# Performance work log

Measured on AMD Instinct MI355X. Metric: run time of the kernel, lower is better.

Reference implementation:

```python
import jax, jax.numpy as jnp
import numpy as np
import math

B, S, D = 1, 4096, 2048
H, KVH, HD = 32, 8, 64
W = 512            # sliding window size (== block size)
THETA = 10000.0
EPS = 1e-5
INTER = 5632
PRE_SCALE = 1.0 / math.sqrt(2.0)


def setup_inputs() -> dict:
    key = jax.random.key(0)
    ks = jax.random.split(key, 8)
    def w(k, shape, fan_in):
        return jax.random.normal(k, shape, jnp.float32) * (fan_in ** -0.5)
    return {
        "hidden_states": jax.random.normal(ks[0], (B, S, D), jnp.float32),
        "mixer_norm_w": jnp.ones((D,), jnp.float32),
        "wq": w(ks[1], (D, H * HD), D),
        "wk": w(ks[2], (D, KVH * HD), D),
        "wv": w(ks[3], (D, KVH * HD), D),
        "wo": w(ks[4], (H * HD, D), H * HD),
        "mlp_norm_w": jnp.ones((D,), jnp.float32),
        "w_gate": w(ks[5], (D, 2 * INTER), D),
        "w_down": w(ks[6], (INTER, D), INTER),
    }


def rmsnorm(x, w, eps=EPS):
    return x * jax.lax.rsqrt(jnp.mean(x * x, axis=-1, keepdims=True) + eps) * w


def rope(x):
    # x: [B, S, h, HD]; rotate-half RoPE
    half = HD // 2
    inv_freq = 1.0 / (THETA ** (jnp.arange(0, HD, 2, dtype=jnp.float32) / HD))
    freqs = jnp.arange(S, dtype=jnp.float32)[:, None] * inv_freq[None, :]  # [S, half]
    cos = jnp.cos(freqs)[None, :, None, :]
    sin = jnp.sin(freqs)[None, :, None, :]
    x1, x2 = x[..., :half], x[..., half:]
    return jnp.concatenate([x1 * cos - x2 * sin, x2 * cos + x1 * sin], axis=-1)


def sliding_attention(x, wq, wk, wv, wo):
    # x already pre-scaled; returns attn output (pre /pre_scale)
    q = (x @ wq).reshape(B, S, H, HD)
    k = (x @ wk).reshape(B, S, KVH, HD)
    v = (x @ wv).reshape(B, S, KVH, HD)
    q, k = rope(q), rope(k)
    rep = H // KVH
    k = jnp.repeat(k, rep, axis=2)  # [B,S,H,HD]
    v = jnp.repeat(v, rep, axis=2)
    nb = S // W
    qb = q.reshape(B, nb, W, H, HD)
    kb = k.reshape(B, nb, W, H, HD)
    vb = v.reshape(B, nb, W, H, HD)
    zeros = jnp.zeros((B, 1, W, H, HD), q.dtype)
    kw = jnp.concatenate([jnp.concatenate([zeros, kb[:, :-1]], axis=1), kb], axis=2)  # [B,nb,2W,H,HD]
    vw = jnp.concatenate([jnp.concatenate([zeros, vb[:, :-1]], axis=1), vb], axis=2)
    # local mask [nb, W, 2W]
    blk = jnp.arange(nb)[:, None, None]
    q_pos = blk * W + jnp.arange(W)[None, :, None]
    k_pos = blk * W - W + jnp.arange(2 * W)[None, None, :]
    mask = (k_pos >= 0) & (k_pos <= q_pos) & (q_pos - k_pos < W)
    scores = jnp.einsum("bnqhd,bnkhd->bhnqk", qb, kw) * (HD ** -0.5)
    scores = jnp.where(mask[None, None], scores, jnp.finfo(scores.dtype).min)
    p = jax.nn.softmax(scores, axis=-1)
    out = jnp.einsum("bhnqk,bnkhd->bnqhd", p, vw).reshape(B, S, H * HD)
    return out @ wo


def reference(hidden_states, mixer_norm_w, wq, wk, wv, wo, mlp_norm_w, w_gate, w_down):
    residual = hidden_states
    x = rmsnorm(hidden_states, mixer_norm_w)
    attn_out = sliding_attention(x * PRE_SCALE, wq, wk, wv, wo) / PRE_SCALE
    h = residual + attn_out
    xn = rmsnorm(h, mlp_norm_w)
    gv = xn @ w_gate
    gate, y = gv[..., :INTER], gv[..., INTER:]
    mlp_out = (jax.nn.silu(gate) * y) @ w_down
    return h + mlp_out
```

## Files before the change

### kernel.cpp

```cpp
#include <hip/hip_runtime.h>
#include <stdint.h>

typedef __attribute__((ext_vector_type(8))) short s16x8;
typedef __attribute__((ext_vector_type(4))) float f32x4;

#define GLD_LDS16(gp, lp) __builtin_amdgcn_global_load_lds( \
    (__attribute__((address_space(1))) void*)(void*)(gp), \
    (__attribute__((address_space(3))) void*)(lp), 16, 0, 0)

__device__ __forceinline__ float b2f(unsigned short s) {
    unsigned int u = ((unsigned int)s) << 16;
    return __builtin_bit_cast(float, u);
}
__device__ __forceinline__ unsigned short f2b(float f) {
    unsigned int u = __builtin_bit_cast(unsigned int, f);
    u = (u + 0x7FFFu + ((u >> 16) & 1u)) >> 16;
    return (unsigned short)u;
}
__device__ __forceinline__ f32x4 mfma16(s16x8 a, s16x8 b, f32x4 c) {
    return __builtin_amdgcn_mfma_f32_16x16x32_bf16(a, b, c, 0, 0, 0);
}

__global__ __launch_bounds__(256) void rmsnorm_bf16(
    const float* __restrict__ x, const float* __restrict__ wgt,
    unsigned short* __restrict__ out)
{
    const int row = blockIdx.x;
    const int t = threadIdx.x;
    const float* xr = x + (size_t)row * 2048;
    float4 a = *(const float4*)(xr + t * 8);
    float4 b = *(const float4*)(xr + t * 8 + 4);
    float ss = a.x*a.x + a.y*a.y + a.z*a.z + a.w*a.w
             + b.x*b.x + b.y*b.y + b.z*b.z + b.w*b.w;
    #pragma unroll
    for (int d = 1; d < 64; d <<= 1) ss += __shfl_xor(ss, d);
    __shared__ float red[4];
    if ((t & 63) == 0) red[t >> 6] = ss;
    __syncthreads();
    float tot = red[0] + red[1] + red[2] + red[3];
    float inv = rsqrtf(tot * (1.0f / 2048.0f) + 1e-5f);
    float vals[8] = {a.x, a.y, a.z, a.w, b.x, b.y, b.z, b.w};
    const float* wr_ = wgt + t * 8;
    s16x8 ov;
    #pragma unroll
    for (int j = 0; j < 8; ++j) ov[j] = (short)f2b(vals[j] * inv * wr_[j]);
    *(s16x8*)(out + (size_t)row * 2048 + t * 8) = ov;
}

__global__ __launch_bounds__(256) void transpose_to_bf16(
    const float* __restrict__ in, unsigned short* __restrict__ out, int K, int N)
{
    __shared__ float tile[64][65];
    const int n0 = blockIdx.x * 64, k0 = blockIdx.y * 64;
    const int t = threadIdx.x;
    const int kr = t >> 4, nc = (t & 15) * 4;
    #pragma unroll
    for (int i = 0; i < 4; ++i) {
        float4 v = *(const float4*)(in + (size_t)(k0 + kr + i * 16) * N + n0 + nc);
        tile[nc + 0][kr + i * 16] = v.x;
        tile[nc + 1][kr + i * 16] = v.y;
        tile[nc + 2][kr + i * 16] = v.z;
        tile[nc + 3][kr + i * 16] = v.w;
    }
    __syncthreads();
    const int nr = t >> 3, kc = (t & 7) * 8;
    #pragma unroll
    for (int p = 0; p < 2; ++p) {
        s16x8 o;
        #pragma unroll
        for (int j = 0; j < 8; ++j) o[j] = (short)f2b(tile[nr + p * 32][kc + j]);
        *(s16x8*)(out + (size_t)(n0 + nr + p * 32) * K + k0 + kc) = o;
    }
}

template <int BN, int EPI>
__global__ __launch_bounds__(512, 2) void gemmq(
    const unsigned short* __restrict__ A,
    const unsigned short* __restrict__ B,
    void* __restrict__ Cv,
    const float* __restrict__ ADD,
    int N, int K)
{
    constexpr int WN  = BN / 4;
    constexpr int HN  = WN / 2;
    constexpr int NJQ = WN / 32;
    constexpr int NBU = BN / 64;
    constexpr int ABUF = 256 * 64;
    constexpr int BBUF = BN * 64;
    __shared__ __align__(16) unsigned short As[2 * ABUF];
    __shared__ __align__(16) unsigned short Bs[2 * BBUF];

    const int t = threadIdx.x;
    const int l = t & 63, w = t >> 6;
    const int l15 = l & 15, lg = l >> 4;
    const int wr = w >> 2, wc = w & 3;
    const int x7 = l15 & 7;
    const int cc0 = ((lg) ^ x7) << 3;
    const int cc1 = ((4 | lg) ^ x7) << 3;

    const int nwg = (int)gridDim.x;
    const int orig = (int)blockIdx.x;
    const int q8 = nwg >> 3, r8 = nwg & 7;
    const int xcd = orig & 7, lid = orig >> 3;
    const int wg = (xcd < r8 ? xcd * (q8 + 1) : r8 * (q8 + 1) + (xcd - r8) * q8) + lid;
    const int m0 = (wg & 15) * 256;
    const int n0 = (wg >> 4) * BN;

    const int tr = t >> 3;
    const int scol = ((t & 7) ^ (tr & 7)) << 3;
    const unsigned short* pA[4];
    #pragma unroll
    for (int u = 0; u < 4; ++u) {
        const int lrow = u * 64 + tr;
        const int g = ((lrow >> 6) & 1) * 128 + (lrow >> 7) * 64 + (lrow & 63);
        pA[u] = A + (size_t)(m0 + g) * K + scol;
    }
    const unsigned short* pB[NBU];
    #pragma unroll
    for (int u = 0; u < NBU; ++u) {
        const int lrow = u * 64 + tr;
        const int h = lrow / (BN / 2), rem = lrow % (BN / 2);
        const int g = (rem / HN) * WN + h * HN + (rem % HN);
        pB[u] = B + (size_t)(n0 + g) * K + scol;
    }

    f32x4 acc[2][2][4][NJQ] = {};
    s16x8 aF[4][2];
    s16x8 bF[2][NJQ][2];

    const int NT = K / 64;

    #pragma unroll
    for (int u = 0; u < 4; ++u) GLD_LDS16(pA[u], &As[u * 4096 + t * 8]);
    #pragma unroll
    for (int u = 0; u < NBU; ++u) GLD_LDS16(pB[u], &Bs[u * 4096 + t * 8]);
    asm volatile("s_waitcnt vmcnt(0)" ::: "memory");
    __builtin_amdgcn_s_barrier();

    for (int kt = 0; kt < NT; ++kt) {
        const int rb  = (kt & 1) ? ABUF : 0;
        const int rbB = (kt & 1) ? BBUF : 0;
        const int wb  = ABUF - rb;
        const int wbB = BBUF - rbB;
        const int knext = (kt + 1 < NT ? kt + 1 : kt) * 64;

        #pragma unroll
        for (int i = 0; i < 4; ++i) {
            const int lr = wr * 64 + i * 16 + l15;
            aF[i][0] = *(const s16x8*)&As[rb + lr * 64 + cc0];
            aF[i][1] = *(const s16x8*)&As[rb + lr * 64 + cc1];
        }
        #pragma unroll
        for (int j = 0; j < NJQ; ++j) {
            const int lr = wc * HN + j * 16 + l15;
            bF[0][j][0] = *(const s16x8*)&Bs[rbB + lr * 64 + cc0];
            bF[0][j][1] = *(const s16x8*)&Bs[rbB + lr * 64 + cc1];
        }
        #pragma unroll
        for (int u = 0; u < 4; ++u)
            GLD_LDS16(pA[u] + knext, &As[wb + u * 4096 + t * 8]);
        __builtin_amdgcn_s_setprio(1);
        #pragma unroll
        for (int kk = 0; kk < 2; ++kk)
            #pragma unroll
            for (int i = 0; i < 4; ++i)
                #pragma unroll
                for (int j = 0; j < NJQ; ++j)
                    acc[0][0][i][j] = mfma16(aF[i][kk], bF[0][j][kk], acc[0][0][i][j]);
        __builtin_amdgcn_s_setprio(0);

        #pragma unroll
        for (int j = 0; j < NJQ; ++j) {
            const int lr = (BN / 2) + wc * HN + j * 16 + l15;
            bF[1][j][0] = *(const s16x8*)&Bs[rbB + lr * 64 + cc0];
            bF[1][j][1] = *(const s16x8*)&Bs[rbB + lr * 64 + cc1];
        }
        #pragma unroll
        for (int u = 0; u < NBU; ++u)
            GLD_LDS16(pB[u] + knext, &Bs[wbB + u * 4096 + t * 8]);
        __builtin_amdgcn_s_setprio(1);
        #pragma unroll
        for (int kk = 0; kk < 2; ++kk)
            #pragma unroll
            for (int i = 0; i < 4; ++i)
                #pragma unroll
                for (int j = 0; j < NJQ; ++j)
                    acc[0][1][i][j] = mfma16(aF[i][kk], bF[1][j][kk], acc[0][1][i][j]);
        __builtin_amdgcn_s_setprio(0);

        #pragma unroll
        for (int i = 0; i < 4; ++i) {
            const int lr = 128 + wr * 64 + i * 16 + l15;
            aF[i][0] = *(const s16x8*)&As[rb + lr * 64 + cc0];
            aF[i][1] = *(const s16x8*)&As[rb + lr * 64 + cc1];
        }
        __builtin_amdgcn_s_setprio(1);
        #pragma unroll
        for (int kk = 0; kk < 2; ++kk)
            #pragma unroll
            for (int i = 0; i < 4; ++i)
                #pragma unroll
                for (int j = 0; j < NJQ; ++j)
                    acc[1][0][i][j] = mfma16(aF[i][kk], bF[0][j][kk], acc[1][0][i][j]);
        __builtin_amdgcn_s_setprio(0);

        __builtin_amdgcn_s_setprio(1);
        #pragma unroll
        for (int kk = 0; kk < 2; ++kk)
            #pragma unroll
            for (int i = 0; i < 4; ++i)
                #pragma unroll
                for (int j = 0; j < NJQ; ++j)
                    acc[1][1][i][j] = mfma16(aF[i][kk], bF[1][j][kk], acc[1][1][i][j]);
        __builtin_amdgcn_s_setprio(0);

        asm volatile("s_waitcnt vmcnt(0)" ::: "memory");
        __builtin_amdgcn_s_barrier();
    }

    #pragma unroll
    for (int qm = 0; qm < 2; ++qm)
        #pragma unroll
        for (int i = 0; i < 4; ++i)
            #pragma unroll
            for (int r = 0; r < 4; ++r) {
                const int row = m0 + wr * 128 + qm * 64 + i * 16 + lg * 4 + r;
                const size_t rbase = (size_t)row * N;
                #pragma unroll
                for (int qn = 0; qn < 2; ++qn)
                    #pragma unroll
                    for (int j = 0; j < NJQ; ++j) {
                        const int col = n0 + wc * WN + qn * HN + j * 16 + l15;
                        float v = acc[qm][qn][i][j][r];
                        if constexpr (EPI == 0) {
                            ((unsigned short*)Cv)[rbase + col] = f2b(v);
                        } else {
                            ((float*)Cv)[rbase + col] = v + ADD[rbase + col];
                        }
                    }
            }
}

__global__ __launch_bounds__(512, 2) void gemm_glu(
    const unsigned short* __restrict__ A,
    const unsigned short* __restrict__ Bg,
    const unsigned short* __restrict__ By,
    unsigned short* __restrict__ act,
    int N, int K)
{
    constexpr int ABUF = 256 * 64, BBUF = 128 * 64;
    __shared__ __align__(16) unsigned short As[2 * ABUF];
    __shared__ __align__(16) unsigned short Bgs[2 * BBUF];
    __shared__ __align__(16) unsigned short Bys[2 * BBUF];

    const int t = threadIdx.x;
    const int l = t & 63, w = t >> 6;
    const int l15 = l & 15, lg = l >> 4;
    const int wr = w >> 2, wc = w & 3;
    const int x7 = l15 & 7;
    const int cc0 = ((lg) ^ x7) << 3;
    const int cc1 = ((4 | lg) ^ x7) << 3;

    const int nwg = (int)gridDim.x;
    const int orig = (int)blockIdx.x;
    const int q8 = nwg >> 3;
    const int xcd = orig & 7, lid = orig >> 3;
    const int wg = xcd * q8 + lid;
    const int m0 = (wg & 15) * 256;
    const int n0 = (wg >> 4) * 128;

    const int tr = t >> 3;
    const int scol = ((t & 7) ^ (tr & 7)) << 3;
    const unsigned short* pA[4];
    #pragma unroll
    for (int u = 0; u < 4; ++u) {
        const int lrow = u * 64 + tr;
        const int g = ((lrow >> 6) & 1) * 128 + (lrow >> 7) * 64 + (lrow & 63);
        pA[u] = A + (size_t)(m0 + g) * K + scol;
    }
    const unsigned short *pG[2], *pY[2];
    #pragma unroll
    for (int u = 0; u < 2; ++u) {
        const int g = (tr >> 4) * 32 + u * 16 + (tr & 15);
        pG[u] = Bg + (size_t)(n0 + g) * K + scol;
        pY[u] = By + (size_t)(n0 + g) * K + scol;
    }

    f32x4 accG[2][2][4] = {};
    f32x4 accY[2][2][4] = {};
    s16x8 aF[4][2];
    s16x8 gF[2][2], yF[2][2];

    const int NT = K / 64;

    #pragma unroll
    for (int u = 0; u < 4; ++u) GLD_LDS16(pA[u], &As[u * 4096 + t * 8]);
    GLD_LDS16(pG[0], &Bgs[0 * 4096 + t * 8]);
    GLD_LDS16(pY[0], &Bys[0 * 4096 + t * 8]);
    GLD_LDS16(pG[1], &Bgs[1 * 4096 + t * 8]);
    GLD_LDS16(pY[1], &Bys[1 * 4096 + t * 8]);
    asm volatile("s_waitcnt vmcnt(0)" ::: "memory");
    __builtin_amdgcn_s_barrier();

    for (int kt = 0; kt < NT; ++kt) {
        const int rb  = (kt & 1) ? ABUF : 0;
        const int rbB = (kt & 1) ? BBUF : 0;
        const int wb  = ABUF - rb;
        const int wbB = BBUF - rbB;
        const int knext = (kt + 1 < NT ? kt + 1 : kt) * 64;

        #pragma unroll
        for (int i = 0; i < 4; ++i) {
            const int lr = wr * 64 + i * 16 + l15;
            aF[i][0] = *(const s16x8*)&As[rb + lr * 64 + cc0];
            aF[i][1] = *(const s16x8*)&As[rb + lr * 64 + cc1];
        }
        {
            const int lr = wc * 16 + l15;
            gF[0][0] = *(const s16x8*)&Bgs[rbB + lr * 64 + cc0];
            gF[0][1] = *(const s16x8*)&Bgs[rbB + lr * 64 + cc1];
            yF[0][0] = *(const s16x8*)&Bys[rbB + lr * 64 + cc0];
            yF[0][1] = *(const s16x8*)&Bys[rbB + lr * 64 + cc1];
        }
        #pragma unroll
        for (int u = 0; u < 4; ++u)
            GLD_LDS16(pA[u] + knext, &As[wb + u * 4096 + t * 8]);
        __builtin_amdgcn_s_setprio(1);
        #pragma unroll
        for (int kk = 0; kk < 2; ++kk)
            #pragma unroll
            for (int i = 0; i < 4; ++i) {
                accG[0][0][i] = mfma16(aF[i][kk], gF[0][kk], accG[0][0][i]);
                accY[0][0][i] = mfma16(aF[i][kk], yF[0][kk], accY[0][0][i]);
            }
        __builtin_amdgcn_s_setprio(0);

        {
            const int lr = 64 + wc * 16 + l15;
            gF[1][0] = *(const s16x8*)&Bgs[rbB + lr * 64 + cc0];
            gF[1][1] = *(const s16x8*)&Bgs[rbB + lr * 64 + cc1];
            yF[1][0] = *(const s16x8*)&Bys[rbB + lr * 64 + cc0];
            yF[1][1] = *(const s16x8*)&Bys[rbB + lr * 64 + cc1];
        }
        GLD_LDS16(pG[0] + knext, &Bgs[wbB + 0 * 4096 + t * 8]);
        GLD_LDS16(pY[0] + knext, &Bys[wbB + 0 * 4096 + t * 8]);
        GLD_LDS16(pG[1] + knext, &Bgs[wbB + 1 * 4096 + t * 8]);
        GLD_LDS16(pY[1] + knext, &Bys[wbB + 1 * 4096 + t * 8]);
        __builtin_amdgcn_s_setprio(1);
        #pragma unroll
        for (int kk = 0; kk < 2; ++kk)
            #pragma unroll
            for (int i = 0; i < 4; ++i) {
                accG[0][1][i] = mfma16(aF[i][kk], gF[1][kk], accG[0][1][i]);
                accY[0][1][i] = mfma16(aF[i][kk], yF[1][kk], accY[0][1][i]);
            }
        __builtin_amdgcn_s_setprio(0);

        #pragma unroll
        for (int i = 0; i < 4; ++i) {
            const int lr = 128 + wr * 64 + i * 16 + l15;
            aF[i][0] = *(const s16x8*)&As[rb + lr * 64 + cc0];
            aF[i][1] = *(const s16x8*)&As[rb + lr * 64 + cc1];
        }
        __builtin_amdgcn_s_setprio(1);
        #pragma unroll
        for (int kk = 0; kk < 2; ++kk)
            #pragma unroll
            for (int i = 0; i < 4; ++i) {
                accG[1][0][i] = mfma16(aF[i][kk], gF[0][kk], accG[1][0][i]);
                accY[1][0][i] = mfma16(aF[i][kk], yF[0][kk], accY[1][0][i]);
            }
        __builtin_amdgcn_s_setprio(0);

        __builtin_amdgcn_s_setprio(1);
        #pragma unroll
        for (int kk = 0; kk < 2; ++kk)
            #pragma unroll
            for (int i = 0; i < 4; ++i) {
                accG[1][1][i] = mfma16(aF[i][kk], gF[1][kk], accG[1][1][i]);
                accY[1][1][i] = mfma16(aF[i][kk], yF[1][kk], accY[1][1][i]);
            }
        __builtin_amdgcn_s_setprio(0);

        asm volatile("s_waitcnt vmcnt(0)" ::: "memory");
        __builtin_amdgcn_s_barrier();
    }

    #pragma unroll
    for (int qm = 0; qm < 2; ++qm)
        #pragma unroll
        for (int i = 0; i < 4; ++i)
            #pragma unroll
            for (int r = 0; r < 4; ++r) {
                const int row = m0 + wr * 128 + qm * 64 + i * 16 + lg * 4 + r;
                const size_t rbase = (size_t)row * N;
                #pragma unroll
                for (int qn = 0; qn < 2; ++qn) {
                    const int col = n0 + wc * 32 + qn * 16 + l15;
                    float g = accG[qm][qn][i][r];
                    float y = accY[qm][qn][i][r];
                    float sg = g / (1.0f + expf(-g));
                    act[rbase + col] = f2b(sg * y);
                }
            }
}

__global__ void rope_tab_k(float2* __restrict__ tab) {
    int i = blockIdx.x * 256 + threadIdx.x;
    if (i >= 4096 * 32) return;
    int s = i >> 5, d = i & 31;
    float inv = exp2f(-(float)d * (13.287712379549449f / 32.0f));
    float fr = (float)s * inv;
    float sv, cv;
    sincosf(fr, &sv, &cv);
    tab[i] = make_float2(cv, sv);
}

__global__ void rope_apply_k(unsigned short* __restrict__ qkv, const float2* __restrict__ tab) {
    int i = blockIdx.x * 256 + threadIdx.x;
    if (i >= 4096 * 40 * 4) return;
    int dg = i & 3;
    int rest = i >> 2;
    int head = rest % 40;
    int s = rest / 40;
    int off = head < 32 ? head * 64 : 2048 + (head - 32) * 64;
    unsigned short* p = qkv + (size_t)s * 3072 + off + dg * 8;
    s16x8 x1 = *(const s16x8*)p;
    s16x8 x2 = *(const s16x8*)(p + 32);
    const float2* tb = tab + s * 32 + dg * 8;
    s16x8 o1, o2;
    #pragma unroll
    for (int j = 0; j < 8; ++j) {
        float2 cs = tb[j];
        float a = b2f((unsigned short)x1[j]);
        float b = b2f((unsigned short)x2[j]);
        o1[j] = (short)f2b(a * cs.x - b * cs.y);
        o2[j] = (short)f2b(b * cs.x + a * cs.y);
    }
    *(s16x8*)p = o1;
    *(s16x8*)(p + 32) = o2;
}

__global__ __launch_bounds__(256) void attn_swa(
    const unsigned short* __restrict__ qkv,
    unsigned short* __restrict__ out)
{
    constexpr int LDQ = 3072;
    const int qb = blockIdx.x;
    const int h = blockIdx.y;
    const int kvh = h >> 2;
    const int q0 = qb * 64;
    const int t = threadIdx.x, l = t & 63, w = t >> 6;
    const int l15 = l & 15, lg = l >> 4;

    __shared__ unsigned short Kl[64 * 64];
    __shared__ unsigned short Vt[64 * 72];
    __shared__ unsigned short Pl[4 * 16 * 72];

    s16x8 qf[2];
    {
        const unsigned short* qp = qkv + (size_t)(q0 + w * 16 + l15) * LDQ + h * 64 + lg * 8;
        qf[0] = *(const s16x8*)(qp);
        qf[1] = *(const s16x8*)(qp + 32);
    }
    float m_run[4] = {-1e30f, -1e30f, -1e30f, -1e30f};
    float l_run[4] = {0.f, 0.f, 0.f, 0.f};
    f32x4 o[4] = {};

    const float SC = 0.0625f * 1.4426950408889634f;
    const int kt_lo = qb >= 8 ? qb - 8 : 0;

    for (int kt = kt_lo; kt <= qb; ++kt) {
        const int ks = kt * 64;
        __syncthreads();
        {
            const unsigned short* kg = qkv + (size_t)(ks + (t >> 3)) * LDQ + 2048 + kvh * 64 + (t & 7) * 8;
            GLD_LDS16(kg, Kl + t * 8);
            GLD_LDS16(kg + (size_t)32 * LDQ, Kl + t * 8 + 2048);
        }
        {
            const unsigned short* vg = qkv + (size_t)(ks + l) * LDQ + 2560 + kvh * 64 + w * 16;
            s16x8 v0 = *(const s16x8*)vg;
            s16x8 v1 = *(const s16x8*)(vg + 8);
            #pragma unroll
            for (int j = 0; j < 8; ++j) Vt[(w * 16 + j) * 72 + l] = (unsigned short)v0[j];
            #pragma unroll
            for (int j = 0; j < 8; ++j) Vt[(w * 16 + 8 + j) * 72 + l] = (unsigned short)v1[j];
        }
        __syncthreads();

        f32x4 sf[4] = {};
        #pragma unroll
        for (int kf = 0; kf < 4; ++kf) {
            #pragma unroll
            for (int kk = 0; kk < 2; ++kk) {
                s16x8 kb = *(const s16x8*)(Kl + (kf * 16 + l15) * 64 + kk * 32 + lg * 8);
                sf[kf] = mfma16(qf[kk], kb, sf[kf]);
            }
        }

        float tmax[4];
        #pragma unroll
        for (int r = 0; r < 4; ++r) {
            int qrow = q0 + w * 16 + lg * 4 + r;
            float mx = -1e30f;
            #pragma unroll
            for (int kf = 0; kf < 4; ++kf) {
                int key = ks + kf * 16 + l15;
                bool valid = (key <= qrow) && (qrow - key < 512);
                if (valid) mx = fmaxf(mx, sf[kf][r]);
            }
            #pragma unroll
            for (int d2 = 1; d2 < 16; d2 <<= 1) mx = fmaxf(mx, __shfl_xor(mx, d2));
            tmax[r] = mx;
        }

        float alpha[4], rsum[4];
        #pragma unroll
        for (int r = 0; r < 4; ++r) {
            float mnew = fmaxf(m_run[r], tmax[r]);
            alpha[r] = exp2f((m_run[r] - mnew) * SC);
            m_run[r] = mnew;
            rsum[r] = 0.f;
        }

        unsigned short* Pw = Pl + w * (16 * 72);
        #pragma unroll
        for (int kf = 0; kf < 4; ++kf) {
            #pragma unroll
            for (int r = 0; r < 4; ++r) {
                int qrow = q0 + w * 16 + lg * 4 + r;
                int key = ks + kf * 16 + l15;
                bool valid = (key <= qrow) && (qrow - key < 512);
                float p = valid ? exp2f((sf[kf][r] - m_run[r]) * SC) : 0.f;
                rsum[r] += p;
                Pw[(lg * 4 + r) * 72 + kf * 16 + l15] = f2b(p);
            }
        }
        #pragma unroll
        for (int r = 0; r < 4; ++r) {
            #pragma unroll
            for (int d2 = 1; d2 < 16; d2 <<= 1) rsum[r] += __shfl_xor(rsum[r], d2);
            l_run[r] = l_run[r] * alpha[r] + rsum[r];
        }
        #pragma unroll
        for (int hf = 0; hf < 4; ++hf)
            #pragma unroll
            for (int r = 0; r < 4; ++r) o[hf][r] *= alpha[r];

        asm volatile("s_waitcnt lgkmcnt(0)" ::: "memory");
        __builtin_amdgcn_sched_barrier(0);

        #pragma unroll
        for (int kk2 = 0; kk2 < 2; ++kk2) {
            s16x8 pa = *(const s16x8*)(Pw + l15 * 72 + kk2 * 32 + lg * 8);
            #pragma unroll
            for (int hf = 0; hf < 4; ++hf) {
                s16x8 vb = *(const s16x8*)(Vt + (hf * 16 + l15) * 72 + kk2 * 32 + lg * 8);
                o[hf] = mfma16(pa, vb, o[hf]);
            }
        }
    }

    #pragma unroll
    for (int r = 0; r < 4; ++r) {
        int qrow = q0 + w * 16 + lg * 4 + r;
        float invl = 1.0f / l_run[r];
        unsigned short* orow = out + (size_t)qrow * 2048 + h * 64;
        #pragma unroll
        for (int hf = 0; hf < 4; ++hf)
            orow[hf * 16 + l15] = f2b(o[hf][r] * invl);
    }
}

extern "C" void kernel_launch(void* const* d_in, const int* in_sizes, int n_in,
                              void* d_out, int out_size, void* d_ws, size_t ws_size,
                              hipStream_t stream)
{
    const float* hidden = (const float*)d_in[0];
    const float* w_mix  = (const float*)d_in[1];
    const float* wq     = (const float*)d_in[2];
    const float* wk     = (const float*)d_in[3];
    const float* wv     = (const float*)d_in[4];
    const float* wo     = (const float*)d_in[5];
    const float* w_mlp  = (const float*)d_in[6];
    const float* wg     = (const float*)d_in[7];
    const float* wd     = (const float*)d_in[8];
    float* out = (float*)d_out;

    char* ws = (char*)d_ws;
    size_t off = 0;
    auto alloc = [&](size_t bytes) {
        char* p = ws + off;
        off += (bytes + 255) & ~(size_t)255;
        return p;
    };
    unsigned short* Wt   = (unsigned short*)alloc((size_t)11264 * 2048 * 2);
    unsigned short* xn   = (unsigned short*)alloc((size_t)4096 * 2048 * 2);
    unsigned short* qkv  = (unsigned short*)alloc((size_t)4096 * 3072 * 2);
    float2*         rtab = (float2*)alloc((size_t)4096 * 32 * 8);
    unsigned short* attn = (unsigned short*)alloc((size_t)4096 * 2048 * 2);
    float*          hbuf = (float*)alloc((size_t)4096 * 2048 * 4);
    unsigned short* act  = (unsigned short*)alloc((size_t)4096 * 5632 * 2);

    rmsnorm_bf16<<<4096, 256, 0, stream>>>(hidden, w_mix, xn);

    transpose_to_bf16<<<dim3(32, 32), 256, 0, stream>>>(wq, Wt, 2048, 2048);
    transpose_to_bf16<<<dim3(8, 32), 256, 0, stream>>>(wk, Wt + (size_t)2048 * 2048, 2048, 512);
    transpose_to_bf16<<<dim3(8, 32), 256, 0, stream>>>(wv, Wt + (size_t)2560 * 2048, 2048, 512);

    gemmq<256, 0><<<192, 512, 0, stream>>>(xn, Wt, qkv, nullptr, 3072, 2048);

    rope_tab_k<<<(4096 * 32 + 255) / 256, 256, 0, stream>>>(rtab);
    rope_apply_k<<<(4096 * 40 * 4 + 255) / 256, 256, 0, stream>>>(qkv, rtab);

    attn_swa<<<dim3(64, 32), 256, 0, stream>>>(qkv, attn);

    transpose_to_bf16<<<dim3(32, 32), 256, 0, stream>>>(wo, Wt, 2048, 2048);
    gemmq<128, 1><<<256, 512, 0, stream>>>(attn, Wt, hbuf, hidden, 2048, 2048);

    rmsnorm_bf16<<<4096, 256, 0, stream>>>(hbuf, w_mlp, xn);

    transpose_to_bf16<<<dim3(176, 32), 256, 0, stream>>>(wg, Wt, 2048, 11264);
    gemm_glu<<<704, 512, 0, stream>>>(xn, Wt, Wt + (size_t)5632 * 2048, act, 5632, 2048);

    transpose_to_bf16<<<dim3(32, 88), 256, 0, stream>>>(wd, Wt, 5632, 2048);
    gemmq<128, 1><<<256, 512, 0, stream>>>(act, Wt, out, hbuf, 2048, 5632);
}
```

Baseline: 534.1 us.

## Fuse RoPE into QKV GEMM epilogue, double-buffer attention K/V, drop setprio

RoPE is now applied in the QKV GEMM epilogue, where each warp holds matching halves of a head (column d and d+32). This removes the separate rope_apply pass over the qkv buffer. The sliding-window attention kernel double-buffers its K/V shared-memory tiles and prefetches the next tile while computing the current one. All s_setprio wrappers around the MFMA blocks in the GEMMs are removed. The costs are extra shared memory in attention and possibly different wave scheduling in the GEMMs without priority hints.

```diff
diff --git a/kernel.cpp b/kernel.cpp
--- a/kernel.cpp
+++ b/kernel.cpp
@@ -79,6 +79,7 @@
     const unsigned short* __restrict__ B,
     void* __restrict__ Cv,
     const float* __restrict__ ADD,
+    const float2* __restrict__ RT,
     int N, int K)
 {
     constexpr int WN  = BN / 4;
@@ -159,7 +160,6 @@
         #pragma unroll
         for (int u = 0; u < 4; ++u)
             GLD_LDS16(pA[u] + knext, &As[wb + u * 4096 + t * 8]);
-        __builtin_amdgcn_s_setprio(1);
         #pragma unroll
         for (int kk = 0; kk < 2; ++kk)
             #pragma unroll
@@ -167,7 +167,6 @@
                 #pragma unroll
                 for (int j = 0; j < NJQ; ++j)
                     acc[0][0][i][j] = mfma16(aF[i][kk], bF[0][j][kk], acc[0][0][i][j]);
-        __builtin_amdgcn_s_setprio(0);
 
         #pragma unroll
         for (int j = 0; j < NJQ; ++j) {
@@ -178,7 +177,6 @@
         #pragma unroll
         for (int u = 0; u < NBU; ++u)
             GLD_LDS16(pB[u] + knext, &Bs[wbB + u * 4096 + t * 8]);
-        __builtin_amdgcn_s_setprio(1);
         #pragma unroll
         for (int kk = 0; kk < 2; ++kk)
             #pragma unroll
@@ -186,7 +184,6 @@
                 #pragma unroll
                 for (int j = 0; j < NJQ; ++j)
                     acc[0][1][i][j] = mfma16(aF[i][kk], bF[1][j][kk], acc[0][1][i][j]);
-        __builtin_amdgcn_s_setprio(0);
 
         #pragma unroll
         for (int i = 0; i < 4; ++i) {
@@ -194,7 +191,6 @@
             aF[i][0] = *(const s16x8*)&As[rb + lr * 64 + cc0];
             aF[i][1] = *(const s16x8*)&As[rb + lr * 64 + cc1];
         }
-        __builtin_amdgcn_s_setprio(1);
         #pragma unroll
         for (int kk = 0; kk < 2; ++kk)
             #pragma unroll
@@ -202,9 +198,7 @@
                 #pragma unroll
                 for (int j = 0; j < NJQ; ++j)
                     acc[1][0][i][j] = mfma16(aF[i][kk], bF[0][j][kk], acc[1][0][i][j]);
-        __builtin_amdgcn_s_setprio(0);
-
-        __builtin_amdgcn_s_setprio(1);
+
         #pragma unroll
         for (int kk = 0; kk < 2; ++kk)
             #pragma unroll
@@ -212,33 +206,61 @@
                 #pragma unroll
                 for (int j = 0; j < NJQ; ++j)
                     acc[1][1][i][j] = mfma16(aF[i][kk], bF[1][j][kk], acc[1][1][i][j]);
-        __builtin_amdgcn_s_setprio(0);
 
         asm volatile("s_waitcnt vmcnt(0)" ::: "memory");
         __builtin_amdgcn_s_barrier();
     }
 
-    #pragma unroll
-    for (int qm = 0; qm < 2; ++qm)
-        #pragma unroll
-        for (int i = 0; i < 4; ++i)
-            #pragma unroll
-            for (int r = 0; r < 4; ++r) {
-                const int row = m0 + wr * 128 + qm * 64 + i * 16 + lg * 4 + r;
-                const size_t rbase = (size_t)row * N;
+    if constexpr (EPI == 2) {
+        unsigned short* Cb = (unsigned short*)Cv;
+        const bool roped = (n0 < 2560);
+        #pragma unroll
+        for (int qm = 0; qm < 2; ++qm)
+            #pragma unroll
+            for (int i = 0; i < 4; ++i)
                 #pragma unroll
-                for (int qn = 0; qn < 2; ++qn)
+                for (int r = 0; r < 4; ++r) {
+                    const int row = m0 + wr * 128 + qm * 64 + i * 16 + lg * 4 + r;
+                    const size_t rbase = (size_t)row * N;
                     #pragma unroll
                     for (int j = 0; j < NJQ; ++j) {
-                        const int col = n0 + wc * WN + qn * HN + j * 16 + l15;
-                        float v = acc[qm][qn][i][j][r];
-                        if constexpr (EPI == 0) {
-                            ((unsigned short*)Cv)[rbase + col] = f2b(v);
+                        const int d = j * 16 + l15;
+                        const int c0 = n0 + wc * WN + j * 16 + l15;
+                        float a = acc[qm][0][i][j][r];
+                        float b = acc[qm][1][i][j][r];
+                        if (roped) {
+                            float2 cs = RT[row * 32 + d];
+                            Cb[rbase + c0]      = f2b(a * cs.x - b * cs.y);
+                            Cb[rbase + c0 + HN] = f2b(b * cs.x + a * cs.y);
                         } else {
-                            ((float*)Cv)[rbase + col] = v + ADD[rbase + col];
+                            Cb[rbase + c0]      = f2b(a);
+                            Cb[rbase + c0 + HN] = f2b(b);
                         }
                     }
-            }
+                }
+    } else {
+        #pragma unroll
+        for (int qm = 0; qm < 2; ++qm)
+            #pragma unroll
+            for (int i = 0; i < 4; ++i)
+                #pragma unroll
+                for (int r = 0; r < 4; ++r) {
+                    const int row = m0 + wr * 128 + qm * 64 + i * 16 + lg * 4 + r;
+                    const size_t rbase = (size_t)row * N;
+                    #pragma unroll
+                    for (int qn = 0; qn < 2; ++qn)
+                        #pragma unroll
+                        for (int j = 0; j < NJQ; ++j) {
+                            const int col = n0 + wc * WN + qn * HN + j * 16 + l15;
+                            float v = acc[qm][qn][i][j][r];
+                            if constexpr (EPI == 0) {
+                                ((unsigned short*)Cv)[rbase + col] = f2b(v);
+                            } else {
+                                ((float*)Cv)[rbase + col] = v + ADD[rbase + col];
+                            }
+                        }
+                }
+    }
 }
 
 __global__ __launch_bounds__(512, 2) void gemm_glu(
@@ -325,7 +347,6 @@
         #pragma unroll
         for (int u = 0; u < 4; ++u)
             GLD_LDS16(pA[u] + knext, &As[wb + u * 4096 + t * 8]);
-        __builtin_amdgcn_s_setprio(1);
         #pragma unroll
         for (int kk = 0; kk < 2; ++kk)
             #pragma unroll
@@ -333,7 +354,6 @@
                 accG[0][0][i] = mfma16(aF[i][kk], gF[0][kk], accG[0][0][i]);
                 accY[0][0][i] = mfma16(aF[i][kk], yF[0][kk], accY[0][0][i]);
             }
-        __builtin_amdgcn_s_setprio(0);
 
         {
             const int lr = 64 + wc * 16 + l15;
@@ -346,7 +366,6 @@
         GLD_LDS16(pY[0] + knext, &Bys[wbB + 0 * 4096 + t * 8]);
         GLD_LDS16(pG[1] + knext, &Bgs[wbB + 1 * 4096 + t * 8]);
         GLD_LDS16(pY[1] + knext, &Bys[wbB + 1 * 4096 + t * 8]);
-        __builtin_amdgcn_s_setprio(1);
         #pragma unroll
         for (int kk = 0; kk < 2; ++kk)
             #pragma unroll
@@ -354,7 +373,6 @@
                 accG[0][1][i] = mfma16(aF[i][kk], gF[1][kk], accG[0][1][i]);
                 accY[0][1][i] = mfma16(aF[i][kk], yF[1][kk], accY[0][1][i]);
             }
-        __builtin_amdgcn_s_setprio(0);
 
         #pragma unroll
         for (int i = 0; i < 4; ++i) {
@@ -362,7 +380,6 @@
             aF[i][0] = *(const s16x8*)&As[rb + lr * 64 + cc0];
             aF[i][1] = *(const s16x8*)&As[rb + lr * 64 + cc1];
         }
-        __builtin_amdgcn_s_setprio(1);
         #pragma unroll
         for (int kk = 0; kk < 2; ++kk)
             #pragma unroll
@@ -370,9 +387,7 @@
                 accG[1][0][i] = mfma16(aF[i][kk], gF[0][kk], accG[1][0][i]);
                 accY[1][0][i] = mfma16(aF[i][kk], yF[0][kk], accY[1][0][i]);
             }
-        __builtin_amdgcn_s_setprio(0);
-
-        __builtin_amdgcn_s_setprio(1);
+
         #pragma unroll
         for (int kk = 0; kk < 2; ++kk)
             #pragma unroll
@@ -380,7 +395,6 @@
                 accG[1][1][i] = mfma16(aF[i][kk], gF[1][kk], accG[1][1][i]);
                 accY[1][1][i] = mfma16(aF[i][kk], yF[1][kk], accY[1][1][i]);
             }
-        __builtin_amdgcn_s_setprio(0);
 
         asm volatile("s_waitcnt vmcnt(0)" ::: "memory");
         __builtin_amdgcn_s_barrier();
@@ -416,31 +430,6 @@
     tab[i] = make_float2(cv, sv);
 }
 
-__global__ void rope_apply_k(unsigned short* __restrict__ qkv, const float2* __restrict__ tab) {
-    int i = blockIdx.x * 256 + threadIdx.x;
-    if (i >= 4096 * 40 * 4) return;
-    int dg = i & 3;
-    int rest = i >> 2;
-    int head = rest % 40;
-    int s = rest / 40;
-    int off = head < 32 ? head * 64 : 2048 + (head - 32) * 64;
-    unsigned short* p = qkv + (size_t)s * 3072 + off + dg * 8;
-    s16x8 x1 = *(const s16x8*)p;
-    s16x8 x2 = *(const s16x8*)(p + 32);
-    const float2* tb = tab + s * 32 + dg * 8;
-    s16x8 o1, o2;
-    #pragma unroll
-    for (int j = 0; j < 8; ++j) {
-        float2 cs = tb[j];
-        float a = b2f((unsigned short)x1[j]);
-        float b = b2f((unsigned short)x2[j]);
-        o1[j] = (short)f2b(a * cs.x - b * cs.y);
-        o2[j] = (short)f2b(b * cs.x + a * cs.y);
-    }
-    *(s16x8*)p = o1;
-    *(s16x8*)(p + 32) = o2;
-}
-
 __global__ __launch_bounds__(256) void attn_swa(
     const unsigned short* __restrict__ qkv,
     unsigned short* __restrict__ out)
@@ -453,8 +442,8 @@
     const int t = threadIdx.x, l = t & 63, w = t >> 6;
     const int l15 = l & 15, lg = l >> 4;
 
-    __shared__ unsigned short Kl[64 * 64];
-    __shared__ unsigned short Vt[64 * 72];
+    __shared__ unsigned short Kl[2][64 * 64];
+    __shared__ unsigned short Vt[2][64 * 72];
     __shared__ unsigned short Pl[4 * 16 * 72];
 
     s16x8 qf[2];
@@ -470,31 +459,45 @@
     const float SC = 0.0625f * 1.4426950408889634f;
     const int kt_lo = qb >= 8 ? qb - 8 : 0;
 
+    {
+        const int ks = kt_lo * 64;
+        const unsigned short* kg = qkv + (size_t)(ks + (t >> 3)) * LDQ + 2048 + kvh * 64 + (t & 7) * 8;
+        GLD_LDS16(kg, &Kl[0][t * 8]);
+        GLD_LDS16(kg + (size_t)32 * LDQ, &Kl[0][t * 8 + 2048]);
+        const unsigned short* vg = qkv + (size_t)(ks + l) * LDQ + 2560 + kvh * 64 + w * 16;
+        s16x8 v0 = *(const s16x8*)vg;
+        s16x8 v1 = *(const s16x8*)(vg + 8);
+        #pragma unroll
+        for (int j = 0; j < 8; ++j) Vt[0][(w * 16 + j) * 72 + l] = (unsigned short)v0[j];
+        #pragma unroll
+        for (int j = 0; j < 8; ++j) Vt[0][(w * 16 + 8 + j) * 72 + l] = (unsigned short)v1[j];
+        asm volatile("s_waitcnt vmcnt(0)" ::: "memory");
+        __syncthreads();
+    }
+
     for (int kt = kt_lo; kt <= qb; ++kt) {
         const int ks = kt * 64;
-        __syncthreads();
-        {
-            const unsigned short* kg = qkv + (size_t)(ks + (t >> 3)) * LDQ + 2048 + kvh * 64 + (t & 7) * 8;
-            GLD_LDS16(kg, Kl + t * 8);
-            GLD_LDS16(kg + (size_t)32 * LDQ, Kl + t * 8 + 2048);
-        }
-        {
-            const unsigned short* vg = qkv + (size_t)(ks + l) * LDQ + 2560 + kvh * 64 + w * 16;
-            s16x8 v0 = *(const s16x8*)vg;
-            s16x8 v1 = *(const s16x8*)(vg + 8);
-            #pragma unroll
-            for (int j = 0; j < 8; ++j) Vt[(w * 16 + j) * 72 + l] = (unsigned short)v0[j];
-            #pragma unroll
-            for (int j = 0; j < 8; ++j) Vt[(w * 16 + 8 + j) * 72 + l] = (unsigned short)v1[j];
-        }
-        __syncthreads();
+        const int cur = (kt - kt_lo) & 1;
+        const int nxt = cur ^ 1;
+        const bool pre = (kt < qb);
+
+        s16x8 v0n, v1n;
+        if (pre) {
+            const int ks1 = ks + 64;
+            const unsigned short* kg = qkv + (size_t)(ks1 + (t >> 3)) * LDQ + 2048 + kvh * 64 + (t & 7) * 8;
+            GLD_LDS16(kg, &Kl[nxt][t * 8]);
+            GLD_LDS16(kg + (size_t)32 * LDQ, &Kl[nxt][t * 8 + 2048]);
+            const unsigned short* vg = qkv + (size_t)(ks1 + l) * LDQ + 2560 + kvh * 64 + w * 16;
+            v0n = *(const s16x8*)vg;
+            v1n = *(const s16x8*)(vg + 8);
+        }
 
         f32x4 sf[4] = {};
         #pragma unroll
         for (int kf = 0; kf < 4; ++kf) {
             #pragma unroll
             for (int kk = 0; kk < 2; ++kk) {
-                s16x8 kb = *(const s16x8*)(Kl + (kf * 16 + l15) * 64 + kk * 32 + lg * 8);
+                s16x8 kb = *(const s16x8*)(&Kl[cur][(kf * 16 + l15) * 64 + kk * 32 + lg * 8]);
                 sf[kf] = mfma16(qf[kk], kb, sf[kf]);
             }
         }
@@ -548,6 +551,13 @@
             #pragma unroll
             for (int r = 0; r < 4; ++r) o[hf][r] *= alpha[r];
 
+        if (pre) {
+            #pragma unroll
+            for (int j = 0; j < 8; ++j) Vt[nxt][(w * 16 + j) * 72 + l] = (unsigned short)v0n[j];
+            #pragma unroll
+            for (int j = 0; j < 8; ++j) Vt[nxt][(w * 16 + 8 + j) * 72 + l] = (unsigned short)v1n[j];
+        }
+
         asm volatile("s_waitcnt lgkmcnt(0)" ::: "memory");
         __builtin_amdgcn_sched_barrier(0);
 
@@ -556,10 +566,13 @@
             s16x8 pa = *(const s16x8*)(Pw + l15 * 72 + kk2 * 32 + lg * 8);
             #pragma unroll
             for (int hf = 0; hf < 4; ++hf) {
-                s16x8 vb = *(const s16x8*)(Vt + (hf * 16 + l15) * 72 + kk2 * 32 + lg * 8);
+                s16x8 vb = *(const s16x8*)(&Vt[cur][(hf * 16 + l15) * 72 + kk2 * 32 + lg * 8]);
                 o[hf] = mfma16(pa, vb, o[hf]);
             }
         }
+
+        asm volatile("s_waitcnt vmcnt(0)" ::: "memory");
+        __syncthreads();
     }
 
     #pragma unroll
@@ -603,21 +616,20 @@
     float*          hbuf = (float*)alloc((size_t)4096 * 2048 * 4);
     unsigned short* act  = (unsigned short*)alloc((size_t)4096 * 5632 * 2);
 
+    rope_tab_k<<<(4096 * 32 + 255) / 256, 256, 0, stream>>>(rtab);
+
     rmsnorm_bf16<<<4096, 256, 0, stream>>>(hidden, w_mix, xn);
 
     transpose_to_bf16<<<dim3(32, 32), 256, 0, stream>>>(wq, Wt, 2048, 2048);
     transpose_to_bf16<<<dim3(8, 32), 256, 0, stream>>>(wk, Wt + (size_t)2048 * 2048, 2048, 512);
     transpose_to_bf16<<<dim3(8, 32), 256, 0, stream>>>(wv, Wt + (size_t)2560 * 2048, 2048, 512);
 
-    gemmq<256, 0><<<192, 512, 0, stream>>>(xn, Wt, qkv, nullptr, 3072, 2048);
-
-    rope_tab_k<<<(4096 * 32 + 255) / 256, 256, 0, stream>>>(rtab);
-    rope_apply_k<<<(4096 * 40 * 4 + 255) / 256, 256, 0, stream>>>(qkv, rtab);
+    gemmq<256, 2><<<192, 512, 0, stream>>>(xn, Wt, qkv, nullptr, rtab, 3072, 2048);
 
     attn_swa<<<dim3(64, 32), 256, 0, stream>>>(qkv, attn);
 
     transpose_to_bf16<<<dim3(32, 32), 256, 0, stream>>>(wo, Wt, 2048, 2048);
-    gemmq<128, 1><<<256, 512, 0, stream>>>(attn, Wt, hbuf, hidden, 2048, 2048);
+    gemmq<128, 1><<<256, 512, 0, stream>>>(attn, Wt, hbuf, hidden, nullptr, 2048, 2048);
 
     rmsnorm_bf16<<<4096, 256, 0, stream>>>(hbuf, w_mlp, xn);
 
@@ -625,5 +637,5 @@
     gemm_glu<<<704, 512, 0, stream>>>(xn, Wt, Wt + (size_t)5632 * 2048, act, 5632, 2048);
 
     transpose_to_bf16<<<dim3(32, 88), 256, 0, stream>>>(wd, Wt, 5632, 2048);
-    gemmq<128, 1><<<256, 512, 0, stream>>>(act, Wt, out, hbuf, 2048, 5632);
-}
+    gemmq<128, 1><<<256, 512, 0, stream>>>(act, Wt, out, hbuf, nullptr, 2048, 5632);
+}
```

New measurement: 584.2 us. 9.4% more time.
